# Kernel optimization log

Hardware: AMD Instinct MI355X
Metric: run time of the kernel (lower is better)

## Reference

```python
import jax, jax.numpy as jnp
import numpy as np

H = 8          # num_channels (heads)
POS = 16       # pos_dim
MAX_F = 16.0
MIN_F = 1.0
HALF_S = 16    # samples_per_dim=32 -> offsets -16..16, S=33
SCALE = POS ** -0.5


def setup_inputs() -> dict:
    key = jax.random.key(0)
    ks = jax.random.split(key, 12)
    B, L, C = 2, 4096, 1024
    p = 0.02
    return {
        'x': jax.random.normal(ks[0], (B, L, C), jnp.float32),
        'wave_w': jax.random.normal(ks[1], (C, 3 * H), jnp.float32) * p,
        'wave_b': jax.random.normal(ks[2], (3 * H,), jnp.float32) * p,
        'query_w': jax.random.normal(ks[3], (C, H * POS), jnp.float32) * p,
        'query_b': jax.random.normal(ks[4], (H * POS,), jnp.float32) * p,
        'key_w': jax.random.normal(ks[5], (POS,), jnp.float32) * p,
        'out_w': jax.random.normal(ks[6], (C, C), jnp.float32) * p,
        'se1_w': jax.random.normal(ks[7], (C, C // 4), jnp.float32) * p,
        'se1_b': jax.random.normal(ks[8], (C // 4,), jnp.float32) * p,
        'se2_w': jax.random.normal(ks[9], (C // 4, C), jnp.float32) * p,
        'se2_b': jax.random.normal(ks[10], (C,), jnp.float32) * p,
    }


def _adaptive_conv(x, wave_w, wave_b, query_w, query_b, key_w, out_w,
                   se1_w, se1_b, se2_w, se2_b):
    B, L, C = x.shape
    D = C // H
    silu = jax.nn.silu
    offsets = jnp.arange(-HALF_S, HALF_S + 1, dtype=x.dtype)  # [S]
    S = offsets.shape[0]

    # wave params -> freq/phase/decay per (B,L,H)
    wave = silu(x @ wave_w + wave_b).reshape(B, L, 3, H)
    freq = jax.nn.sigmoid(wave[:, :, 0, :]) * (MAX_F - MIN_F) + MIN_F
    phase = jnp.tanh(wave[:, :, 1, :]) * MAX_F
    decay = jax.nn.sigmoid(wave[:, :, 2, :]) * 9.5 + 0.5
    queries = silu(x @ query_w + query_b).reshape(B, L, H, POS)

    freq_avg = freq.mean(axis=-1)    # [B,L]
    phase_avg = phase.mean(axis=-1)  # [B,L]

    centers = jnp.arange(L, dtype=x.dtype)
    # [B,L,S] real-valued sample positions
    sample_pos = (centers[None, :, None]
                  + offsets[None, None, :] * freq_avg[..., None]
                  + phase_avg[..., None])
    valid = (sample_pos >= 0) & (sample_pos < L)           # [B,L,S]
    sample_idx = jnp.clip(sample_pos.astype(jnp.int32), 0, L - 1)

    # gather: values[b,l,s,:] = x[b, sample_idx[b,l,s], :]
    values = jnp.take_along_axis(x, sample_idx.reshape(B, L * S, 1), axis=1)
    values = values.reshape(B, L, S, H, D).transpose(0, 1, 3, 2, 4)  # [B,L,H,S,D]

    rel = jnp.abs(offsets)[None, None, None, :] * freq[..., None]    # [B,L,H,S]
    keys = silu(rel[..., None] * key_w)                              # [B,L,H,S,POS]
    logits = jnp.einsum('blhd,blhsd->blhs', queries, keys) * SCALE

    vmask = valid[:, :, None, :]                                     # [B,L,H,S]
    logits = jnp.where(vmask, logits, -1e30)
    env = jnp.exp(-rel / jnp.maximum(decay[..., None], 0.1))
    w = jax.nn.softmax(logits, axis=-1) * env * vmask.astype(x.dtype)
    w = w / (w.sum(axis=-1, keepdims=True) + 1e-8)

    out = jnp.einsum('blhsd,blhs->blhd', values, w).reshape(B, L, C)
    se = jax.nn.sigmoid(silu(out @ se1_w + se1_b) @ se2_w + se2_b)
    out = out * se
    return silu(out @ out_w)


def reference(x, wave_w, wave_b, query_w, query_b, key_w, out_w,
              se1_w, se1_b, se2_w, se2_b):
    return _adaptive_conv(x, wave_w, wave_b, query_w, query_b, key_w,
                          out_w, se1_w, se1_b, se2_w, se2_b)
```

## Files before the change

kernel.cpp:

```cpp
#include <hip/hip_runtime.h>
#include <math.h>

#define HN 8
#define POSN 16
#define SN 33
#define HALF_SN 16
#define CDIM 1024
#define LDIM 4096
#define BDIM 2
#define NTOK (BDIM * LDIM)

typedef unsigned short u16;
typedef short short8 __attribute__((ext_vector_type(8)));
typedef u16 u16x8 __attribute__((ext_vector_type(8)));
typedef unsigned int u32x4 __attribute__((ext_vector_type(4)));
typedef float f32x4 __attribute__((ext_vector_type(4)));

__device__ __forceinline__ float sigf(float x) { return 1.0f / (1.0f + expf(-x)); }
__device__ __forceinline__ float siluf(float x) { return x / (1.0f + expf(-x)); }
__device__ __forceinline__ float frcp(float x) { return __builtin_amdgcn_rcpf(x); }
__device__ __forceinline__ float fexp(float x) { return __expf(x); }
__device__ __forceinline__ float fsig(float x) { return frcp(1.0f + fexp(-x)); }
__device__ __forceinline__ float fsilu(float x) { return x * fsig(x); }

__device__ __forceinline__ u16 f2b(float f) {
    union { float f; unsigned u; } v; v.f = f;
    unsigned r = v.u + 0x7fffu + ((v.u >> 16) & 1u);
    return (u16)(r >> 16);
}
__device__ __forceinline__ float b2f(u16 v) {
    union { unsigned u; float f; } x; x.u = ((unsigned)v) << 16; return x.f;
}
__device__ __forceinline__ float u2f(unsigned u) {
    union { unsigned u; float f; } x; x.u = u; return x.f;
}
__device__ __forceinline__ void ld_lds16(const void* g, void* l) {
    __builtin_amdgcn_global_load_lds(
        (const __attribute__((address_space(1))) void*)g,
        (__attribute__((address_space(3))) void*)l, 16, 0, 0);
}

__global__ __launch_bounds__(256) void xcast(
    const float* __restrict__ x, u16* __restrict__ xb)
{
    const int i = blockIdx.x * 256 + threadIdx.x;
    float4 a = ((const float4*)x)[(size_t)i * 2];
    float4 b = ((const float4*)x)[(size_t)i * 2 + 1];
    u16x8 o;
    o[0]=f2b(a.x); o[1]=f2b(a.y); o[2]=f2b(a.z); o[3]=f2b(a.w);
    o[4]=f2b(b.x); o[5]=f2b(b.y); o[6]=f2b(b.z); o[7]=f2b(b.w);
    ((u16x8*)xb)[i] = o;
}

__global__ __launch_bounds__(256) void transcast(
    const float* __restrict__ in, u16* __restrict__ out, int N, int K)
{
    __shared__ float tile[32][33];
    const int bn = blockIdx.x * 32, bk = blockIdx.y * 32;
    const int tx = threadIdx.x & 31, ty = threadIdx.x >> 5;
    #pragma unroll
    for (int yy = ty; yy < 32; yy += 8)
        tile[yy][tx] = in[(size_t)(bk + yy) * N + bn + tx];
    __syncthreads();
    #pragma unroll
    for (int yy = ty; yy < 32; yy += 8)
        out[(size_t)(bn + yy) * K + bk + tx] = f2b(tile[tx][yy]);
}

__global__ __launch_bounds__(256) void wave_kernel(
    const float* __restrict__ x, const float* __restrict__ wave_w,
    const float* __restrict__ wave_b, float* __restrict__ freq,
    float* __restrict__ decay, float* __restrict__ favg, float* __restrict__ pavg)
{
    const int tid = threadIdx.x;
    const int tok = tid >> 5, col = tid & 31;
    const int t = blockIdx.x * 8 + tok;
    __shared__ float wsct[24][260];
    __shared__ float wsh[8][24];
    __shared__ float fsh[8][8], psh[8][8];

    const float* xrow = x + (size_t)t * CDIM;
    float acc = (col < 24) ? wave_b[col] : 0.0f;

    for (int k0 = 0; k0 < CDIM; k0 += 256) {
        __syncthreads();
        {
            const float* wr = wave_w + (size_t)(k0 + tid) * 24;
            float4 w0 = *(const float4*)(wr + 0);
            float4 w1 = *(const float4*)(wr + 4);
            float4 w2 = *(const float4*)(wr + 8);
            float4 w3 = *(const float4*)(wr + 12);
            float4 w4 = *(const float4*)(wr + 16);
            float4 w5 = *(const float4*)(wr + 20);
            wsct[0][tid]=w0.x;  wsct[1][tid]=w0.y;  wsct[2][tid]=w0.z;  wsct[3][tid]=w0.w;
            wsct[4][tid]=w1.x;  wsct[5][tid]=w1.y;  wsct[6][tid]=w1.z;  wsct[7][tid]=w1.w;
            wsct[8][tid]=w2.x;  wsct[9][tid]=w2.y;  wsct[10][tid]=w2.z; wsct[11][tid]=w2.w;
            wsct[12][tid]=w3.x; wsct[13][tid]=w3.y; wsct[14][tid]=w3.z; wsct[15][tid]=w3.w;
            wsct[16][tid]=w4.x; wsct[17][tid]=w4.y; wsct[18][tid]=w4.z; wsct[19][tid]=w4.w;
            wsct[20][tid]=w5.x; wsct[21][tid]=w5.y; wsct[22][tid]=w5.z; wsct[23][tid]=w5.w;
        }
        __syncthreads();
        if (col < 24) {
            #pragma unroll 4
            for (int kk = 0; kk < 256; kk += 4) {
                float4 xv = *(const float4*)(xrow + k0 + kk);
                float4 wv = *(const float4*)(&wsct[col][kk]);
                acc += xv.x * wv.x; acc += xv.y * wv.y;
                acc += xv.z * wv.z; acc += xv.w * wv.w;
            }
        }
    }
    if (col < 24) wsh[tok][col] = siluf(acc);
    __syncthreads();
    if (col < 8) {
        float f = sigf(wsh[tok][col])      * 15.0f + 1.0f;
        float p = tanhf(wsh[tok][8 + col]) * 16.0f;
        float d = sigf(wsh[tok][16 + col]) * 9.5f + 0.5f;
        freq[(size_t)t * HN + col] = f;
        decay[(size_t)t * HN + col] = d;
        fsh[tok][col] = f; psh[tok][col] = p;
    }
    __syncthreads();
    if (col == 0) {
        float fa = 0.f, pa = 0.f;
        for (int h = 0; h < HN; ++h) { fa += fsh[tok][h]; pa += psh[tok][h]; }
        favg[t] = fa * 0.125f; pavg[t] = pa * 0.125f;
    }
}

template <int MODE, int CFG>
__global__ __launch_bounds__(256) void mfma_gemm(
    const u16* __restrict__ A, const u16* __restrict__ Bt,
    const float* __restrict__ bias, const u16* __restrict__ mulb,
    void* __restrict__ Cptr, int M, int N, int K)
{
    constexpr int BM  = (CFG == 0) ? 128 : 32;
    constexpr int MI  = (CFG == 0) ? 4 : 2;
    constexpr int NJ  = (CFG == 0) ? 4 : 2;
    constexpr int ACH = BM / 16;
    constexpr int NCH = ACH + 8;

    __shared__ u16 lds[2][(BM + 128) * 32];

    const int nwg = gridDim.x * gridDim.y;
    const int flat = blockIdx.y * gridDim.x + blockIdx.x;
    const int swz = (flat & 7) * (nwg >> 3) + (flat >> 3);
    const int bxi = swz / gridDim.y, byi = swz % gridDim.y;

    const int tid = threadIdx.x;
    const int bm = bxi * BM, bn = byi * 128;
    const int wid = tid >> 6, lane = tid & 63;
    const int wr = (CFG == 0) ? (wid >> 1) * 64 : 0;
    const int wc = (CFG == 0) ? (wid & 1) * 64 : wid * 32;
    const int fm = lane & 15;
    const int kg = (lane >> 4) * 8;
    const int lrow = lane >> 2;
    const int lk   = (lane & 3) * 8;

    f32x4 acc[MI][NJ];
    #pragma unroll
    for (int i = 0; i < MI; ++i)
        #pragma unroll
        for (int j = 0; j < NJ; ++j) acc[i][j] = (f32x4){0.f, 0.f, 0.f, 0.f};

    auto stage = [&](u16* dst, int k0s) {
        #pragma unroll
        for (int c = wid; c < NCH; c += 4) {
            const u16* gsrc = (c < ACH)
                ? A  + (size_t)(bm + c * 16 + lrow) * K + k0s + lk
                : Bt + (size_t)(bn + (c - ACH) * 16 + lrow) * K + k0s + lk;
            ld_lds16(gsrc, dst + c * 512 + lane * 8);
        }
    };

    stage(&lds[0][0], 0);
    __syncthreads();
    int cur = 0;
    for (int k0 = 0; k0 < K; k0 += 32) {
        const int k1 = (k0 + 32 < K) ? (k0 + 32) : k0;
        stage(&lds[cur ^ 1][0], k1);
        short8 a[MI], b[NJ];
        #pragma unroll
        for (int i = 0; i < MI; ++i)
            a[i] = *(const short8*)&lds[cur][(wr + i * 16 + fm) * 32 + kg];
        #pragma unroll
        for (int j = 0; j < NJ; ++j)
            b[j] = *(const short8*)&lds[cur][(BM + wc + j * 16 + fm) * 32 + kg];
        #pragma unroll
        for (int i = 0; i < MI; ++i)
            #pragma unroll
            for (int j = 0; j < NJ; ++j)
                acc[i][j] = __builtin_amdgcn_mfma_f32_16x16x32_bf16(a[i], b[j], acc[i][j], 0, 0, 0);
        __syncthreads();
        cur ^= 1;
    }

    float* Cf = (float*)Cptr;
    u16* Cb = (u16*)Cptr;
    #pragma unroll
    for (int i = 0; i < MI; ++i) {
        const int row0 = bm + wr + i * 16 + (lane >> 4) * 4;
        #pragma unroll
        for (int j = 0; j < NJ; ++j) {
            const int col = bn + wc + j * 16 + fm;
            const float vb = (MODE == 3) ? 0.0f : bias[col];
            #pragma unroll
            for (int e = 0; e < 4; ++e) {
                const int row = row0 + e;
                float v = acc[i][j][e];
                if (MODE == 0 || MODE == 1) v = fsilu(v + vb);
                if (MODE == 2) v = fsig(v + vb) * b2f(mulb[(size_t)row * N + col]);
                if (MODE == 3) v = fsilu(v);
                if (MODE == 0 || MODE == 3) Cf[(size_t)row * N + col] = v;
                else                        Cb[(size_t)row * N + col] = f2b(v);
            }
        }
    }
}

__global__ __launch_bounds__(256) void adaptconv_kernel(
    const u16* __restrict__ xbf, const float* __restrict__ key_w,
    const float* __restrict__ q, const float* __restrict__ freq,
    const float* __restrict__ decay, const float* __restrict__ favg,
    const float* __restrict__ pavg, u16* __restrict__ out)
{
    const int bid = blockIdx.x;
    const int swz = (bid & 7) * (NTOK / 16) + (bid >> 3);
    const int sub = threadIdx.x >> 7, lt = threadIdx.x & 127;
    const int t = swz * 2 + sub;
    const int b = t / LDIM, l = t % LDIM;
    const int h = lt >> 4;
    const int li = lt & 15;

    __shared__ float qs[2][HN][17];
    __shared__ float kw[POSN];
    __shared__ float fr[2][HN], dc[2][HN];
    __shared__ int   boff[2][SN];
    __shared__ float msk[2][SN];
    __shared__ float vsh[2][HN][17];
    __shared__ float esh[2][HN][17];
    __shared__ float wgt[2][HN][SN];

    qs[sub][lt >> 4][lt & 15] = q[(size_t)t * 128 + lt];
    if (threadIdx.x < POSN) kw[threadIdx.x] = key_w[threadIdx.x];
    if (lt < HN) {
        fr[sub][lt] = freq[(size_t)t * HN + lt];
        dc[sub][lt] = decay[(size_t)t * HN + lt];
    }
    if (lt < SN) {
        float fa = favg[t], pa = pavg[t];
        float sp = (float)l + (float)(lt - HALF_SN) * fa + pa;
        bool v = (sp >= 0.0f) && (sp < (float)LDIM);
        int si = (int)sp;
        si = min(max(si, 0), LDIM - 1);
        boff[sub][lt] = si * (CDIM * 2);
        msk[sub][lt] = v ? 1.0f : 0.0f;
    }
    __syncthreads();

    {
        const float fh = fr[sub][h];
        const float rdci = frcp(fmaxf(dc[sub][h], 0.1f));
        for (int ds = li; ds < 17; ds += 16) {
            float rel = (float)ds * fh;
            float acc = 0.0f;
            #pragma unroll
            for (int p = 0; p < POSN; ++p)
                acc += qs[sub][h][p] * fsilu(rel * kw[p]);
            vsh[sub][h][ds] = 0.25f * acc;
            esh[sub][h][ds] = fexp(-rel * rdci);
        }
    }
    __syncthreads();

    {
        const int ns = (li == 0) ? 3 : 2;
        int   sI[3] = { li, li + 16, 32 };
        float lg[3];
        #pragma unroll
        for (int k = 0; k < 3; ++k) {
            if (k < ns) {
                const int s = sI[k], ds = abs(s - 16);
                lg[k] = (msk[sub][s] != 0.0f) ? vsh[sub][h][ds] : -1e30f;
            } else lg[k] = -3.4e38f;
        }
        float m = fmaxf(lg[0], fmaxf(lg[1], lg[2]));
        #pragma unroll
        for (int d = 1; d < 16; d <<= 1) m = fmaxf(m, __shfl_xor(m, d));

        float e[3]; float ssum = 0.0f;
        #pragma unroll
        for (int k = 0; k < 3; ++k) {
            e[k] = (k < ns) ? fexp(lg[k] - m) : 0.0f;
            ssum += e[k];
        }
        #pragma unroll
        for (int d = 1; d < 16; d <<= 1) ssum += __shfl_xor(ssum, d);

        const float rss = frcp(ssum);
        float wv[3]; float wsum = 0.0f;
        #pragma unroll
        for (int k = 0; k < 3; ++k) {
            if (k < ns) {
                const int s = sI[k], ds = abs(s - 16);
                wv[k] = e[k] * rss * esh[sub][h][ds] * msk[sub][s];
            } else wv[k] = 0.0f;
            wsum += wv[k];
        }
        #pragma unroll
        for (int d = 1; d < 16; d <<= 1) wsum += __shfl_xor(wsum, d);

        const float inv = frcp(wsum + 1e-8f);
        #pragma unroll
        for (int k = 0; k < 3; ++k)
            if (k < ns) wgt[sub][h][sI[k]] = wv[k] * inv;
    }
    __syncthreads();

    const char* xbB = (const char*)(xbf + (size_t)b * LDIM * CDIM);
    const int cbyte = lt * 16;
    float a0=0,a1=0,a2=0,a3=0,a4=0,a5=0,a6=0,a7=0;

    #define GFMA(V, W) do { \
        a0 += (W) * u2f((V)[0] << 16); a1 += (W) * u2f((V)[0] & 0xffff0000u); \
        a2 += (W) * u2f((V)[1] << 16); a3 += (W) * u2f((V)[1] & 0xffff0000u); \
        a4 += (W) * u2f((V)[2] << 16); a5 += (W) * u2f((V)[2] & 0xffff0000u); \
        a6 += (W) * u2f((V)[3] << 16); a7 += (W) * u2f((V)[3] & 0xffff0000u); } while (0)

    int s = 0;
    for (; s + 4 <= SN; s += 4) {
        u32x4 v0 = *(const u32x4*)(xbB + boff[sub][s]     + cbyte);
        u32x4 v1 = *(const u32x4*)(xbB + boff[sub][s + 1] + cbyte);
        u32x4 v2 = *(const u32x4*)(xbB + boff[sub][s + 2] + cbyte);
        u32x4 v3 = *(const u32x4*)(xbB + boff[sub][s + 3] + cbyte);
        float w0 = wgt[sub][h][s],     w1 = wgt[sub][h][s + 1];
        float w2 = wgt[sub][h][s + 2], w3 = wgt[sub][h][s + 3];
        GFMA(v0, w0); GFMA(v1, w1); GFMA(v2, w2); GFMA(v3, w3);
    }
    for (; s < SN; ++s) {
        u32x4 v = *(const u32x4*)(xbB + boff[sub][s] + cbyte);
        float w = wgt[sub][h][s];
        GFMA(v, w);
    }
    #undef GFMA

    u16x8 o;
    o[0]=f2b(a0); o[1]=f2b(a1); o[2]=f2b(a2); o[3]=f2b(a3);
    o[4]=f2b(a4); o[5]=f2b(a5); o[6]=f2b(a6); o[7]=f2b(a7);
    *(u16x8*)(out + (size_t)t * CDIM + lt * 8) = o;
}

extern "C" void kernel_launch(void* const* d_in, const int* in_sizes, int n_in,
                              void* d_out, int out_size, void* d_ws, size_t ws_size,
                              hipStream_t stream)
{
    const float* x       = (const float*)d_in[0];
    const float* wave_w  = (const float*)d_in[1];
    const float* wave_b  = (const float*)d_in[2];
    const float* query_w = (const float*)d_in[3];
    const float* query_b = (const float*)d_in[4];
    const float* key_w   = (const float*)d_in[5];
    const float* out_w   = (const float*)d_in[6];
    const float* se1_w   = (const float*)d_in[7];
    const float* se1_b   = (const float*)d_in[8];
    const float* se2_w   = (const float*)d_in[9];
    const float* se2_b   = (const float*)d_in[10];

    char* wsb = (char*)d_ws;
    float* q     = (float*)wsb;         wsb += (size_t)NTOK * 128 * 4;
    float* freq  = (float*)wsb;         wsb += (size_t)NTOK * HN * 4;
    float* decay = (float*)wsb;         wsb += (size_t)NTOK * HN * 4;
    float* favg  = (float*)wsb;         wsb += (size_t)NTOK * 4;
    float* pavg  = (float*)wsb;         wsb += (size_t)NTOK * 4;
    u16* x_bf    = (u16*)wsb;           wsb += (size_t)NTOK * CDIM * 2;
    u16* conv_bf = (u16*)wsb;           wsb += (size_t)NTOK * CDIM * 2;
    u16* tmp1_bf = (u16*)wsb;           wsb += (size_t)NTOK * 256 * 2;
    u16* g_bf    = (u16*)wsb;           wsb += (size_t)NTOK * CDIM * 2;
    u16* qw_bf   = (u16*)wsb;           wsb += (size_t)128 * CDIM * 2;
    u16* se1w_bf = (u16*)wsb;           wsb += (size_t)256 * CDIM * 2;
    u16* se2w_bf = (u16*)wsb;           wsb += (size_t)CDIM * 256 * 2;
    u16* outw_bf = (u16*)wsb;           wsb += (size_t)CDIM * CDIM * 2;

    xcast<<<NTOK * CDIM / 8 / 256, 256, 0, stream>>>(x, x_bf);
    transcast<<<dim3(128 / 32, CDIM / 32), 256, 0, stream>>>(query_w, qw_bf, 128, CDIM);
    transcast<<<dim3(256 / 32, CDIM / 32), 256, 0, stream>>>(se1_w, se1w_bf, 256, CDIM);
    transcast<<<dim3(CDIM / 32, 256 / 32), 256, 0, stream>>>(se2_w, se2w_bf, CDIM, 256);
    transcast<<<dim3(CDIM / 32, CDIM / 32), 256, 0, stream>>>(out_w, outw_bf, CDIM, CDIM);

    wave_kernel<<<NTOK / 8, 256, 0, stream>>>(x, wave_w, wave_b, freq, decay, favg, pavg);

    mfma_gemm<0, 1><<<dim3(NTOK / 32, 1), 256, 0, stream>>>(
        x_bf, qw_bf, query_b, nullptr, q, NTOK, 128, CDIM);

    adaptconv_kernel<<<NTOK / 2, 256, 0, stream>>>(
        x_bf, key_w, q, freq, decay, favg, pavg, conv_bf);

    mfma_gemm<1, 1><<<dim3(NTOK / 32, 256 / 128), 256, 0, stream>>>(
        conv_bf, se1w_bf, se1_b, nullptr, tmp1_bf, NTOK, 256, CDIM);

    mfma_gemm<2, 0><<<dim3(NTOK / 128, CDIM / 128), 256, 0, stream>>>(
        tmp1_bf, se2w_bf, se2_b, conv_bf, g_bf, NTOK, CDIM, 256);

    mfma_gemm<3, 0><<<dim3(NTOK / 128, CDIM / 128), 256, 0, stream>>>(
        g_bf, outw_bf, nullptr, nullptr, d_out, NTOK, CDIM, CDIM);
}
```

Baseline: 156.0 us.

## Fuse x bf16 cast into wave kernel, merge weight transcasts, store q as bf16

```diff
diff --git a/kernel.cpp b/kernel.cpp
--- a/kernel.cpp
+++ b/kernel.cpp
@@ -40,23 +40,22 @@
         (__attribute__((address_space(3))) void*)l, 16, 0, 0);
 }
 
-__global__ __launch_bounds__(256) void xcast(
-    const float* __restrict__ x, u16* __restrict__ xb)
+__global__ __launch_bounds__(256) void transcast_all(
+    const float* __restrict__ qw, const float* __restrict__ s1,
+    const float* __restrict__ s2, const float* __restrict__ ow,
+    u16* __restrict__ oq, u16* __restrict__ o1,
+    u16* __restrict__ o2, u16* __restrict__ oo)
 {
-    const int i = blockIdx.x * 256 + threadIdx.x;
-    float4 a = ((const float4*)x)[(size_t)i * 2];
-    float4 b = ((const float4*)x)[(size_t)i * 2 + 1];
-    u16x8 o;
-    o[0]=f2b(a.x); o[1]=f2b(a.y); o[2]=f2b(a.z); o[3]=f2b(a.w);
-    o[4]=f2b(b.x); o[5]=f2b(b.y); o[6]=f2b(b.z); o[7]=f2b(b.w);
-    ((u16x8*)xb)[i] = o;
-}
-
-__global__ __launch_bounds__(256) void transcast(
-    const float* __restrict__ in, u16* __restrict__ out, int N, int K)
-{
+    const int bid = blockIdx.x;
+    const float* in; u16* out; int N, K, base;
+    if      (bid < 128) { in = qw; out = oq; N = 128;  K = 1024; base = 0;   }
+    else if (bid < 384) { in = s1; out = o1; N = 256;  K = 1024; base = 128; }
+    else if (bid < 640) { in = s2; out = o2; N = 1024; K = 256;  base = 384; }
+    else                { in = ow; out = oo; N = 1024; K = 1024; base = 640; }
+    const int rel = bid - base, nx = N / 32;
+    const int bn = (rel % nx) * 32, bk = (rel / nx) * 32;
+
     __shared__ float tile[32][33];
-    const int bn = blockIdx.x * 32, bk = blockIdx.y * 32;
     const int tx = threadIdx.x & 31, ty = threadIdx.x >> 5;
     #pragma unroll
     for (int yy = ty; yy < 32; yy += 8)
@@ -69,15 +68,28 @@
 
 __global__ __launch_bounds__(256) void wave_kernel(
     const float* __restrict__ x, const float* __restrict__ wave_w,
-    const float* __restrict__ wave_b, float* __restrict__ freq,
-    float* __restrict__ decay, float* __restrict__ favg, float* __restrict__ pavg)
+    const float* __restrict__ wave_b, u16* __restrict__ xbf,
+    float* __restrict__ freq, float* __restrict__ decay,
+    float* __restrict__ favg, float* __restrict__ pavg)
 {
     const int tid = threadIdx.x;
     const int tok = tid >> 5, col = tid & 31;
-    const int t = blockIdx.x * 8 + tok;
+    const int t0 = blockIdx.x * 8;
+    const int t = t0 + tok;
     __shared__ float wsct[24][260];
     __shared__ float wsh[8][24];
     __shared__ float fsh[8][8], psh[8][8];
+
+    for (int i = tid; i < 1024; i += 256) {
+        const int r = i >> 7, c8 = (i & 127) * 8;
+        const float* src = x + (size_t)(t0 + r) * CDIM + c8;
+        float4 a = *(const float4*)(src);
+        float4 b = *(const float4*)(src + 4);
+        u16x8 o;
+        o[0]=f2b(a.x); o[1]=f2b(a.y); o[2]=f2b(a.z); o[3]=f2b(a.w);
+        o[4]=f2b(b.x); o[5]=f2b(b.y); o[6]=f2b(b.z); o[7]=f2b(b.w);
+        *(u16x8*)(xbf + (size_t)(t0 + r) * CDIM + c8) = o;
+    }
 
     const float* xrow = x + (size_t)t * CDIM;
     float acc = (col < 24) ? wave_b[col] : 0.0f;
@@ -208,11 +220,11 @@
             for (int e = 0; e < 4; ++e) {
                 const int row = row0 + e;
                 float v = acc[i][j][e];
-                if (MODE == 0 || MODE == 1) v = fsilu(v + vb);
+                if (MODE == 1) v = fsilu(v + vb);
                 if (MODE == 2) v = fsig(v + vb) * b2f(mulb[(size_t)row * N + col]);
                 if (MODE == 3) v = fsilu(v);
-                if (MODE == 0 || MODE == 3) Cf[(size_t)row * N + col] = v;
-                else                        Cb[(size_t)row * N + col] = f2b(v);
+                if (MODE == 3) Cf[(size_t)row * N + col] = v;
+                else           Cb[(size_t)row * N + col] = f2b(v);
             }
         }
     }
@@ -220,7 +232,7 @@
 
 __global__ __launch_bounds__(256) void adaptconv_kernel(
     const u16* __restrict__ xbf, const float* __restrict__ key_w,
-    const float* __restrict__ q, const float* __restrict__ freq,
+    const u16* __restrict__ qb, const float* __restrict__ freq,
     const float* __restrict__ decay, const float* __restrict__ favg,
     const float* __restrict__ pavg, u16* __restrict__ out)
 {
@@ -241,7 +253,7 @@
     __shared__ float esh[2][HN][17];
     __shared__ float wgt[2][HN][SN];
 
-    qs[sub][lt >> 4][lt & 15] = q[(size_t)t * 128 + lt];
+    qs[sub][lt >> 4][lt & 15] = b2f(qb[(size_t)t * 128 + lt]);
     if (threadIdx.x < POSN) kw[threadIdx.x] = key_w[threadIdx.x];
     if (lt < HN) {
         fr[sub][lt] = freq[(size_t)t * HN + lt];
@@ -367,7 +379,7 @@
     const float* se2_b   = (const float*)d_in[10];
 
     char* wsb = (char*)d_ws;
-    float* q     = (float*)wsb;         wsb += (size_t)NTOK * 128 * 4;
+    u16* q_bf    = (u16*)wsb;           wsb += (size_t)NTOK * 128 * 2;
     float* freq  = (float*)wsb;         wsb += (size_t)NTOK * HN * 4;
     float* decay = (float*)wsb;         wsb += (size_t)NTOK * HN * 4;
     float* favg  = (float*)wsb;         wsb += (size_t)NTOK * 4;
@@ -381,19 +393,17 @@
     u16* se2w_bf = (u16*)wsb;           wsb += (size_t)CDIM * 256 * 2;
     u16* outw_bf = (u16*)wsb;           wsb += (size_t)CDIM * CDIM * 2;
 
-    xcast<<<NTOK * CDIM / 8 / 256, 256, 0, stream>>>(x, x_bf);
-    transcast<<<dim3(128 / 32, CDIM / 32), 256, 0, stream>>>(query_w, qw_bf, 128, CDIM);
-    transcast<<<dim3(256 / 32, CDIM / 32), 256, 0, stream>>>(se1_w, se1w_bf, 256, CDIM);
-    transcast<<<dim3(CDIM / 32, 256 / 32), 256, 0, stream>>>(se2_w, se2w_bf, CDIM, 256);
-    transcast<<<dim3(CDIM / 32, CDIM / 32), 256, 0, stream>>>(out_w, outw_bf, CDIM, CDIM);
-
-    wave_kernel<<<NTOK / 8, 256, 0, stream>>>(x, wave_w, wave_b, freq, decay, favg, pavg);
-
-    mfma_gemm<0, 1><<<dim3(NTOK / 32, 1), 256, 0, stream>>>(
-        x_bf, qw_bf, query_b, nullptr, q, NTOK, 128, CDIM);
+    transcast_all<<<1664, 256, 0, stream>>>(
+        query_w, se1_w, se2_w, out_w, qw_bf, se1w_bf, se2w_bf, outw_bf);
+
+    wave_kernel<<<NTOK / 8, 256, 0, stream>>>(
+        x, wave_w, wave_b, x_bf, freq, decay, favg, pavg);
+
+    mfma_gemm<1, 1><<<dim3(NTOK / 32, 1), 256, 0, stream>>>(
+        x_bf, qw_bf, query_b, nullptr, q_bf, NTOK, 128, CDIM);
 
     adaptconv_kernel<<<NTOK / 2, 256, 0, stream>>>(
-        x_bf, key_w, q, freq, decay, favg, pavg, conv_bf);
+        x_bf, key_w, q_bf, freq, decay, favg, pavg, conv_bf);
 
     mfma_gemm<1, 1><<<dim3(NTOK / 32, 256 / 128), 256, 0, stream>>>(
         conv_bf, se1w_bf, se1_b, nullptr, tmp1_bf, NTOK, 256, CDIM);
```

Measured after the change: 145.7 us. 6.6% less time.
